# Performance work log

Hardware: AMD Instinct MI355X
Metric: run time of the kernel (lower is better)

The kernel has to match this reference:

```python
import jax, jax.numpy as jnp
import numpy as np

B, T, D, DO = 8, 2048, 1024, 1024

def setup_inputs() -> dict:
    key = jax.random.key(0)
    ks = jax.random.split(key, 7)
    s = 1.0 / np.sqrt(D)
    return {
        "input_tensor": jax.random.normal(ks[0], (B, T, D), dtype=jnp.float32),
        "Wq": jax.random.uniform(ks[1], (D, D), jnp.float32, -s, s),
        "bq": jax.random.uniform(ks[2], (D,), jnp.float32, -s, s),
        "Wk": jax.random.uniform(ks[3], (D, D), jnp.float32, -s, s),
        "bk": jax.random.uniform(ks[4], (D,), jnp.float32, -s, s),
        "Wv": jax.random.uniform(ks[5], (D, DO), jnp.float32, -s, s),
        "bv": jax.random.uniform(ks[6], (DO,), jnp.float32, -s, s),
    }

def reference(input_tensor, Wq, bq, Wk, bk, Wv, bv):
    scale = jnp.sqrt(jnp.float32(input_tensor.shape[-1]))
    q = input_tensor @ Wq + bq            # [B,T,D]
    k = input_tensor @ Wk + bk            # [B,T,D]
    v = input_tensor @ Wv + bv            # [B,T,DO]
    scores = jnp.einsum('btd,bsd->bts', q, k) / scale  # [B,T,T]
    attn = jax.nn.softmax(scores, axis=-1)
    return jnp.einsum('bts,bso->bto', attn, v)         # [B,T,DO]
```

## Files before the change

kernel.cpp:

```cpp
#include <hip/hip_runtime.h>
#include <stdint.h>

typedef unsigned short u16;
typedef __attribute__((ext_vector_type(4))) float    floatx4;
typedef __attribute__((ext_vector_type(8))) __bf16   bf16x8;
typedef __attribute__((ext_vector_type(4))) unsigned int uintx4;

__device__ inline u16 f2bf(float f) {
  unsigned int u = __builtin_bit_cast(unsigned int, f);
  u += 0x7fffu + ((u >> 16) & 1u);
  return (u16)(u >> 16);
}

#define GLD16(gsrc, ldst)                                                        \
  __builtin_amdgcn_global_load_lds(                                              \
      (__attribute__((address_space(1))) void*)(gsrc),                           \
      (__attribute__((address_space(3))) void*)(ldst), 16, 0, 0)

__global__ __launch_bounds__(256) void cast_x_kernel(const float* __restrict__ x,
                                                     u16* __restrict__ xb) {
  long i = ((long)blockIdx.x * 256 + threadIdx.x) * 8;
  floatx4 a = *(const floatx4*)(x + i);
  floatx4 b = *(const floatx4*)(x + i + 4);
  uintx4 o;
  o[0] = (unsigned)f2bf(a[0]) | ((unsigned)f2bf(a[1]) << 16);
  o[1] = (unsigned)f2bf(a[2]) | ((unsigned)f2bf(a[3]) << 16);
  o[2] = (unsigned)f2bf(b[0]) | ((unsigned)f2bf(b[1]) << 16);
  o[3] = (unsigned)f2bf(b[2]) | ((unsigned)f2bf(b[3]) << 16);
  *(uintx4*)(xb + i) = o;
}

__global__ __launch_bounds__(256) void transpose_cast_w(const float* __restrict__ Wq,
                                                        const float* __restrict__ Wk,
                                                        const float* __restrict__ Wv,
                                                        u16* __restrict__ WT) {
  __shared__ float tile[32][33];
  const int z = blockIdx.z;
  const float* W = (z == 0) ? Wq : (z == 1) ? Wk : Wv;
  u16* dst = WT + (long)z * 1024 * 1024;
  int bx = blockIdx.x * 32, by = blockIdx.y * 32;
  int tx = threadIdx.x, ty = threadIdx.y;
  for (int i = 0; i < 32; i += 8)
    tile[ty + i][tx] = W[(long)(by + ty + i) * 1024 + bx + tx];
  __syncthreads();
  for (int i = 0; i < 32; i += 8)
    dst[(long)(bx + ty + i) * 1024 + by + tx] = f2bf(tile[tx][ty + i]);
}

#define BM 128
#define BN 128
#define BK 64

template <int MODE, int GN>
__global__ __launch_bounds__(256, 2)
void gemm_bt(const u16* __restrict__ Aall, const u16* __restrict__ Ball,
             void* __restrict__ Call, void* __restrict__ C2,
             const float* __restrict__ bias, const float* __restrict__ bias2,
             float* __restrict__ lsum,
             int M, int N, int K, long aStride, long bStride, long cStride) {
  __shared__ __align__(16) u16 As[BM * BK];
  __shared__ __align__(16) u16 Bs[BN * BK];

  const int z = blockIdx.z;
  const u16* A  = Aall + (long)z * aStride;
  const u16* Bt = Ball + (long)z * bStride;

  int m_idx, n_idx;
  if (GN > 0) {
    const int tiles_n = gridDim.x, tiles_m = gridDim.y;
    int bid = blockIdx.y * tiles_n + blockIdx.x;
    int per_group = GN * tiles_m;
    int g = bid / per_group;
    int rem = bid - g * per_group;
    n_idx = g * GN + rem % GN;
    m_idx = rem / GN;
  } else {
    m_idx = blockIdx.y; n_idx = blockIdx.x;
  }

  const int tid  = threadIdx.x;
  const int m0   = m_idx * BM;
  const int n0   = n_idx * BN;
  const int wave = tid >> 6;
  const int lane = tid & 63;
  const int wm   = (wave & 1) * 64;
  const int wn   = (wave >> 1) * 64;
  const int l15  = lane & 15;
  const int quad = lane >> 4;

  floatx4 acc[4][4];
  floatx4 zero = {0.f, 0.f, 0.f, 0.f};
  for (int i = 0; i < 4; ++i)
    for (int j = 0; j < 4; ++j) acc[i][j] = zero;

  int srow[4], scol[4], sdst[4];
  for (int i = 0; i < 4; ++i) {
    int ci = i * 256 + tid;
    int r = ci >> 3, sc = ci & 7;
    srow[i] = r;
    scol[i] = (sc ^ (r & 7)) * 8;
    sdst[i] = ci * 8;
  }

  for (int kt = 0; kt < K; kt += BK) {
#pragma unroll
    for (int i = 0; i < 4; ++i) {
      GLD16(A  + (long)(m0 + srow[i]) * K + kt + scol[i], As + sdst[i]);
      GLD16(Bt + (long)(n0 + srow[i]) * K + kt + scol[i], Bs + sdst[i]);
    }
    __syncthreads();
#pragma unroll
    for (int ks = 0; ks < 2; ++ks) {
      bf16x8 af[4], bfr[4];
#pragma unroll
      for (int mi = 0; mi < 4; ++mi) {
        int r = wm + mi * 16 + l15;
        int ch = r * 8 + ((ks * 4 + quad) ^ (r & 7));
        af[mi] = *(const bf16x8*)(As + ch * 8);
      }
#pragma unroll
      for (int ni = 0; ni < 4; ++ni) {
        int r = wn + ni * 16 + l15;
        int ch = r * 8 + ((ks * 4 + quad) ^ (r & 7));
        bfr[ni] = *(const bf16x8*)(Bs + ch * 8);
      }
#pragma unroll
      for (int mi = 0; mi < 4; ++mi)
#pragma unroll
        for (int ni = 0; ni < 4; ++ni)
          acc[mi][ni] = __builtin_amdgcn_mfma_f32_16x16x32_bf16(
              af[mi], bfr[ni], acc[mi][ni], 0, 0, 0);
    }
    __syncthreads();
  }

#pragma unroll
  for (int mi = 0; mi < 4; ++mi) {
    const int row = m0 + wm + mi * 16 + quad * 4;
    if (MODE == 2) {
      u16* C = (u16*)Call + (long)z * cStride;
      float rs[4] = {0.f, 0.f, 0.f, 0.f};
#pragma unroll
      for (int ni = 0; ni < 4; ++ni) {
        int col = n0 + wn + ni * 16 + l15;
        floatx4 v = acc[mi][ni];
#pragma unroll
        for (int r = 0; r < 4; ++r) {
          float e = __expf(v[r] * 0.03125f);
          C[(long)(row + r) * N + col] = f2bf(e);
          rs[r] += e;
        }
      }
#pragma unroll
      for (int r = 0; r < 4; ++r) {
        float t = rs[r];
        t += __shfl_xor(t, 1);
        t += __shfl_xor(t, 2);
        t += __shfl_xor(t, 4);
        t += __shfl_xor(t, 8);
        if (l15 == 0) atomicAdd(lsum + (long)z * 2048 + row + r, t);
      }
    } else if (MODE == 3) {
      float* C = (float*)Call + (long)z * cStride;
      const float* lz = lsum + (long)z * 2048;
      floatx4 lv = *(const floatx4*)(lz + row);
      float inv[4];
#pragma unroll
      for (int r = 0; r < 4; ++r) inv[r] = 1.0f / lv[r];
#pragma unroll
      for (int ni = 0; ni < 4; ++ni) {
        int col = n0 + wn + ni * 16 + l15;
        floatx4 v = acc[mi][ni];
#pragma unroll
        for (int r = 0; r < 4; ++r)
          C[(long)(row + r) * N + col] = v[r] * inv[r];
      }
    } else if (MODE == 0) {
#pragma unroll
      for (int ni = 0; ni < 4; ++ni) {
        int col = n0 + wn + ni * 16 + l15;
        u16* C = (col < 1024) ? (u16*)Call : (u16*)C2;
        float b = (col < 1024) ? bias[col] : bias2[col - 1024];
        int c = col & 1023;
        floatx4 v = acc[mi][ni];
#pragma unroll
        for (int r = 0; r < 4; ++r)
          C[(long)(row + r) * 1024 + c] = f2bf(v[r] + b);
      }
    } else {
      u16* C = (u16*)Call;
#pragma unroll
      for (int ni = 0; ni < 4; ++ni) {
        int col = n0 + wn + ni * 16 + l15;
        long base = ((long)(col >> 11) * 1024) * 2048 + (col & 2047);
        floatx4 v = acc[mi][ni];
#pragma unroll
        for (int r = 0; r < 4; ++r)
          C[base + (long)(row + r) * 2048] = f2bf(v[r] + bias[row + r]);
      }
    }
  }
}

extern "C" void kernel_launch(void* const* d_in, const int* in_sizes, int n_in,
                              void* d_out, int out_size, void* d_ws, size_t ws_size,
                              hipStream_t stream) {
  const float* x  = (const float*)d_in[0];
  const float* Wq = (const float*)d_in[1];
  const float* bq = (const float*)d_in[2];
  const float* Wk = (const float*)d_in[3];
  const float* bk = (const float*)d_in[4];
  const float* Wv = (const float*)d_in[5];
  const float* bv = (const float*)d_in[6];
  float* out = (float*)d_out;

  const long BT = 16384;
  u16* xb = (u16*)d_ws;
  u16* WT = xb + BT * 1024;
  u16* qb = WT + 3L * 1024 * 1024;
  u16* kb = qb + BT * 1024;
  u16* vT = kb + BT * 1024;
  u16* S  = vT + BT * 1024;
  float* lsum = (float*)(S + 8L * 2048 * 2048);

  hipMemsetAsync(lsum, 0, 8 * 2048 * sizeof(float), stream);

  cast_x_kernel<<<8192, 256, 0, stream>>>(x, xb);
  transpose_cast_w<<<dim3(32, 32, 3), dim3(32, 8), 0, stream>>>(Wq, Wk, Wv, WT);

  gemm_bt<0, 8><<<dim3(16, 128, 1), 256, 0, stream>>>(
      xb, WT, qb, kb, bq, bk, nullptr, 16384, 2048, 1024, 0, 0, 0);
  gemm_bt<1, 8><<<dim3(128, 8, 1), 256, 0, stream>>>(
      WT + 2L * 1024 * 1024, xb, vT, nullptr, bv, nullptr, nullptr,
      1024, 16384, 1024, 0, 0, 0);
  gemm_bt<2, 8><<<dim3(16, 16, 8), 256, 0, stream>>>(
      qb, kb, S, nullptr, nullptr, nullptr, lsum,
      2048, 2048, 1024, 2048L * 1024, 2048L * 1024, 2048L * 2048);
  gemm_bt<3, 8><<<dim3(8, 16, 8), 256, 0, stream>>>(
      S, vT, out, nullptr, nullptr, nullptr, lsum,
      2048, 1024, 2048, 2048L * 2048, 1024L * 2048, 2048L * 1024);
}
```

Measured before the change: 427.5 us.

## Swap MFMA operands for row-contiguous epilogue stores and merge prep kernels

Swaps the A/B operands of the MFMA so each lane holds four consecutive columns of one row. All GEMM epilogues can then write vectorized 8- or 16-byte chunks instead of scattered 2- or 4-byte stores, and the softmax row-sum needs fewer shuffles and atomics. Separately, the x cast and weight transpose-cast kernels are merged into one launch to save a launch. The risks are that the operand swap changes accumulator layout semantics, which must match the epilogue indexing, and that the merged kernel has uneven block types.

```diff
diff --git a/kernel.cpp b/kernel.cpp
--- a/kernel.cpp
+++ b/kernel.cpp
@@ -4,6 +4,7 @@
 typedef unsigned short u16;
 typedef __attribute__((ext_vector_type(4))) float    floatx4;
 typedef __attribute__((ext_vector_type(8))) __bf16   bf16x8;
+typedef __attribute__((ext_vector_type(2))) unsigned int uintx2;
 typedef __attribute__((ext_vector_type(4))) unsigned int uintx4;
 
 __device__ inline u16 f2bf(float f) {
@@ -17,25 +18,28 @@
       (__attribute__((address_space(1))) void*)(gsrc),                           \
       (__attribute__((address_space(3))) void*)(ldst), 16, 0, 0)
 
-__global__ __launch_bounds__(256) void cast_x_kernel(const float* __restrict__ x,
-                                                     u16* __restrict__ xb) {
-  long i = ((long)blockIdx.x * 256 + threadIdx.x) * 8;
-  floatx4 a = *(const floatx4*)(x + i);
-  floatx4 b = *(const floatx4*)(x + i + 4);
-  uintx4 o;
-  o[0] = (unsigned)f2bf(a[0]) | ((unsigned)f2bf(a[1]) << 16);
-  o[1] = (unsigned)f2bf(a[2]) | ((unsigned)f2bf(a[3]) << 16);
-  o[2] = (unsigned)f2bf(b[0]) | ((unsigned)f2bf(b[1]) << 16);
-  o[3] = (unsigned)f2bf(b[2]) | ((unsigned)f2bf(b[3]) << 16);
-  *(uintx4*)(xb + i) = o;
-}
-
-__global__ __launch_bounds__(256) void transpose_cast_w(const float* __restrict__ Wq,
-                                                        const float* __restrict__ Wk,
-                                                        const float* __restrict__ Wv,
-                                                        u16* __restrict__ WT) {
+__global__ __launch_bounds__(256) void prep_kernel(const float* __restrict__ x,
+                                                   const float* __restrict__ Wq,
+                                                   const float* __restrict__ Wk,
+                                                   const float* __restrict__ Wv,
+                                                   u16* __restrict__ xb,
+                                                   u16* __restrict__ WT) {
+  const int z = blockIdx.z;
+  const int tid = threadIdx.y * 32 + threadIdx.x;
+  if (z >= 3) {
+    long blk = (long)(z - 3) * 1024 + blockIdx.y * 32 + blockIdx.x;
+    long i = (blk * 256 + tid) * 8;
+    floatx4 a = *(const floatx4*)(x + i);
+    floatx4 b = *(const floatx4*)(x + i + 4);
+    uintx4 o;
+    o[0] = (unsigned)f2bf(a[0]) | ((unsigned)f2bf(a[1]) << 16);
+    o[1] = (unsigned)f2bf(a[2]) | ((unsigned)f2bf(a[3]) << 16);
+    o[2] = (unsigned)f2bf(b[0]) | ((unsigned)f2bf(b[1]) << 16);
+    o[3] = (unsigned)f2bf(b[2]) | ((unsigned)f2bf(b[3]) << 16);
+    *(uintx4*)(xb + i) = o;
+    return;
+  }
   __shared__ float tile[32][33];
-  const int z = blockIdx.z;
   const float* W = (z == 0) ? Wq : (z == 1) ? Wk : Wv;
   u16* dst = WT + (long)z * 1024 * 1024;
   int bx = blockIdx.x * 32, by = blockIdx.y * 32;
@@ -129,74 +133,67 @@
 #pragma unroll
         for (int ni = 0; ni < 4; ++ni)
           acc[mi][ni] = __builtin_amdgcn_mfma_f32_16x16x32_bf16(
-              af[mi], bfr[ni], acc[mi][ni], 0, 0, 0);
+              bfr[ni], af[mi], acc[mi][ni], 0, 0, 0);
     }
     __syncthreads();
   }
 
 #pragma unroll
   for (int mi = 0; mi < 4; ++mi) {
-    const int row = m0 + wm + mi * 16 + quad * 4;
+    const int row = m0 + wm + mi * 16 + l15;
     if (MODE == 2) {
       u16* C = (u16*)Call + (long)z * cStride;
-      float rs[4] = {0.f, 0.f, 0.f, 0.f};
-#pragma unroll
-      for (int ni = 0; ni < 4; ++ni) {
-        int col = n0 + wn + ni * 16 + l15;
-        floatx4 v = acc[mi][ni];
-#pragma unroll
-        for (int r = 0; r < 4; ++r) {
-          float e = __expf(v[r] * 0.03125f);
-          C[(long)(row + r) * N + col] = f2bf(e);
-          rs[r] += e;
-        }
-      }
-#pragma unroll
-      for (int r = 0; r < 4; ++r) {
-        float t = rs[r];
-        t += __shfl_xor(t, 1);
-        t += __shfl_xor(t, 2);
-        t += __shfl_xor(t, 4);
-        t += __shfl_xor(t, 8);
-        if (l15 == 0) atomicAdd(lsum + (long)z * 2048 + row + r, t);
-      }
+      float rs = 0.f;
+#pragma unroll
+      for (int ni = 0; ni < 4; ++ni) {
+        int colb = n0 + wn + ni * 16 + quad * 4;
+        floatx4 v = acc[mi][ni];
+        float e0 = __expf(v[0] * 0.03125f), e1 = __expf(v[1] * 0.03125f);
+        float e2 = __expf(v[2] * 0.03125f), e3 = __expf(v[3] * 0.03125f);
+        rs += (e0 + e1) + (e2 + e3);
+        uintx2 o;
+        o[0] = (unsigned)f2bf(e0) | ((unsigned)f2bf(e1) << 16);
+        o[1] = (unsigned)f2bf(e2) | ((unsigned)f2bf(e3) << 16);
+        *(uintx2*)(C + (long)row * N + colb) = o;
+      }
+      rs += __shfl_xor(rs, 16);
+      rs += __shfl_xor(rs, 32);
+      if (quad == 0) atomicAdd(lsum + (long)z * 2048 + row, rs);
     } else if (MODE == 3) {
       float* C = (float*)Call + (long)z * cStride;
-      const float* lz = lsum + (long)z * 2048;
-      floatx4 lv = *(const floatx4*)(lz + row);
-      float inv[4];
-#pragma unroll
-      for (int r = 0; r < 4; ++r) inv[r] = 1.0f / lv[r];
-#pragma unroll
-      for (int ni = 0; ni < 4; ++ni) {
-        int col = n0 + wn + ni * 16 + l15;
-        floatx4 v = acc[mi][ni];
-#pragma unroll
-        for (int r = 0; r < 4; ++r)
-          C[(long)(row + r) * N + col] = v[r] * inv[r];
+      float inv = 1.0f / lsum[(long)z * 2048 + row];
+#pragma unroll
+      for (int ni = 0; ni < 4; ++ni) {
+        int colb = n0 + wn + ni * 16 + quad * 4;
+        floatx4 v = acc[mi][ni];
+        floatx4 o = {v[0] * inv, v[1] * inv, v[2] * inv, v[3] * inv};
+        *(floatx4*)(C + (long)row * N + colb) = o;
       }
     } else if (MODE == 0) {
 #pragma unroll
       for (int ni = 0; ni < 4; ++ni) {
-        int col = n0 + wn + ni * 16 + l15;
-        u16* C = (col < 1024) ? (u16*)Call : (u16*)C2;
-        float b = (col < 1024) ? bias[col] : bias2[col - 1024];
-        int c = col & 1023;
-        floatx4 v = acc[mi][ni];
-#pragma unroll
-        for (int r = 0; r < 4; ++r)
-          C[(long)(row + r) * 1024 + c] = f2bf(v[r] + b);
+        int colb = n0 + wn + ni * 16 + quad * 4;
+        u16* C = (colb < 1024) ? (u16*)Call : (u16*)C2;
+        const float* bp = (colb < 1024) ? bias + colb : bias2 + (colb - 1024);
+        floatx4 b = *(const floatx4*)bp;
+        floatx4 v = acc[mi][ni];
+        uintx2 o;
+        o[0] = (unsigned)f2bf(v[0] + b[0]) | ((unsigned)f2bf(v[1] + b[1]) << 16);
+        o[1] = (unsigned)f2bf(v[2] + b[2]) | ((unsigned)f2bf(v[3] + b[3]) << 16);
+        *(uintx2*)(C + (long)row * 1024 + (colb & 1023)) = o;
       }
     } else {
       u16* C = (u16*)Call;
-#pragma unroll
-      for (int ni = 0; ni < 4; ++ni) {
-        int col = n0 + wn + ni * 16 + l15;
-        long base = ((long)(col >> 11) * 1024) * 2048 + (col & 2047);
-        floatx4 v = acc[mi][ni];
-#pragma unroll
-        for (int r = 0; r < 4; ++r)
-          C[base + (long)(row + r) * 2048] = f2bf(v[r] + bias[row + r]);
+      float b = bias[row];
+#pragma unroll
+      for (int ni = 0; ni < 4; ++ni) {
+        int colb = n0 + wn + ni * 16 + quad * 4;
+        long base = ((long)(colb >> 11) * 1024) * 2048 + (colb & 2047);
+        floatx4 v = acc[mi][ni];
+        uintx2 o;
+        o[0] = (unsigned)f2bf(v[0] + b) | ((unsigned)f2bf(v[1] + b) << 16);
+        o[1] = (unsigned)f2bf(v[2] + b) | ((unsigned)f2bf(v[3] + b) << 16);
+        *(uintx2*)(C + base + (long)row * 2048) = o;
       }
     }
   }
@@ -225,8 +222,7 @@
 
   hipMemsetAsync(lsum, 0, 8 * 2048 * sizeof(float), stream);
 
-  cast_x_kernel<<<8192, 256, 0, stream>>>(x, xb);
-  transpose_cast_w<<<dim3(32, 32, 3), dim3(32, 8), 0, stream>>>(Wq, Wk, Wv, WT);
+  prep_kernel<<<dim3(32, 32, 11), dim3(32, 8), 0, stream>>>(x, Wq, Wk, Wv, xb, WT);
 
   gemm_bt<0, 8><<<dim3(16, 128, 1), 256, 0, stream>>>(
       xb, WT, qb, kb, bq, bk, nullptr, 16384, 2048, 1024, 0, 0, 0);
```

Measured after the change: 426.9 us. About the same (-0.1%).
